# Kernel optimization log

Measured on AMD Instinct MI355X. Metric: run time of the kernel, lower is better.

The kernel has to match this reference:

```python
import jax, jax.numpy as jnp
import numpy as np

B, IN, H, OUT = 4096, 1024, 2048, 1024
EPS = 1e-5  # added to std (not variance), matching the torch module


def _ln(z, a, b):
    # torch.std default is unbiased (ddof=1); eps added to sigma
    mu = jnp.mean(z, axis=1, keepdims=True)
    sigma = jnp.std(z, axis=1, ddof=1, keepdims=True)
    return (z - mu) / (sigma + EPS) * a + b


def setup_inputs() -> dict:
    key = jax.random.key(0)
    ks = iter(jax.random.split(key, 40))
    W = lambda i, o: (jax.random.normal(next(ks), (o, i), jnp.float32) / np.sqrt(i)).astype(jnp.float32)
    bz = lambda o: jnp.zeros((o,), jnp.float32)
    d = {
        "inp": jax.random.normal(next(ks), (B, IN), jnp.float32),
        "h_0": jax.random.normal(next(ks), (B, H), jnp.float32),
        "c_0": jax.random.normal(next(ks), (B, H), jnp.float32),
        # h-side gate linears (H -> H)
        "Wfh": W(H, H), "bfh": bz(H), "Wih": W(H, H), "bih": bz(H),
        "Wch": W(H, H), "bch": bz(H), "Woh": W(H, H), "boh": bz(H),
        # x-side gate linears (IN -> H)
        "Wfx": W(IN, H), "bfx": bz(H), "Wix": W(IN, H), "bix": bz(H),
        "Wcx": W(IN, H), "bcx": bz(H), "Wox": W(IN, H), "box": bz(H),
        # decoder (H -> OUT)
        "Wdec": W(H, OUT), "bdec": bz(OUT),
        # LayerNormalization params (a2 ones, b2 zeros), shape (1, H)
        "ax": jnp.ones((1, H), jnp.float32), "bx": jnp.zeros((1, H), jnp.float32),
        "ah": jnp.ones((1, H), jnp.float32), "bh": jnp.zeros((1, H), jnp.float32),
        "ac": jnp.ones((1, H), jnp.float32), "bc": jnp.zeros((1, H), jnp.float32),
    }
    return d


def reference(inp, h_0, c_0,
              Wfh, bfh, Wih, bih, Wch, bch, Woh, boh,
              Wfx, bfx, Wix, bix, Wcx, bcx, Wox, box,
              Wdec, bdec, ax, bx, ah, bh, ac, bc):
    lin = lambda x, W, b: x @ W.T + b
    gate = lambda wx, bx_, wh, bh_: (_ln(lin(inp, wx, bx_), ax, bx)
                                     + _ln(lin(h_0, wh, bh_), ah, bh))
    f_g = jax.nn.sigmoid(gate(Wfx, bfx, Wfh, bfh))
    i_g = jax.nn.sigmoid(gate(Wix, bix, Wih, bih))
    c_tilda = jnp.tanh(gate(Wcx, bcx, Wch, bch))
    cx = f_g * c_0 + i_g * c_tilda
    o_g = jax.nn.sigmoid(gate(Wox, box, Woh, boh))
    hx = o_g * jnp.tanh(_ln(cx, ac, bc))
    out = lin(hx, Wdec, bdec)  # decoder applied to hidden state (vectorized over batch)
    return (out, hx, cx)
```

## Files before the change

kernel.cpp:

```cpp
#include <hip/hip_runtime.h>

#define NB   4096
#define NIN  1024
#define NH   2048
#define NOUT 1024
#define NH4  8192

typedef short short8 __attribute__((ext_vector_type(8)));
typedef float f32x4 __attribute__((ext_vector_type(4)));
typedef float f32x16 __attribute__((ext_vector_type(16)));
typedef unsigned short ushort8v __attribute__((ext_vector_type(8)));

__device__ __forceinline__ float bf2f(unsigned short u) {
  union { unsigned int i; float f; } c; c.i = ((unsigned int)u) << 16; return c.f;
}
__device__ __forceinline__ unsigned short f2bf(float f) {
  union { float f; unsigned int i; } c; c.f = f;
  unsigned int u = c.i;
  u += 0x7FFFu + ((u >> 16) & 1u);
  return (unsigned short)(u >> 16);
}
__device__ __forceinline__ float sigf(float x) { return 1.0f / (1.0f + __expf(-x)); }
__device__ __forceinline__ float tanh_f(float x) { return 1.0f - 2.0f / (__expf(2.0f * x) + 1.0f); }

#define CNT_INP  ((size_t)NB * NIN)
#define CNT_H0   ((size_t)NB * NH)
#define CNT_WXG  ((size_t)NH * NIN)
#define CNT_WHG  ((size_t)NH * NH)
#define CNT_WD   ((size_t)NOUT * NH)
#define OFF_XB   ((size_t)0)
#define OFF_H0B  (OFF_XB + CNT_INP)
#define OFF_HXB  (OFF_H0B + CNT_H0)
#define OFF_WX   (OFF_HXB + CNT_H0)
#define OFF_WH   (OFF_WX + 4 * CNT_WXG)
#define OFF_WD   (OFF_WH + 4 * CNT_WHG)
#define OFF_ZX   (OFF_WD + CNT_WD)
#define OFF_ZH   (OFF_ZX + (size_t)NB * NH4)
#define CVT_TOTAL (OFF_WD + CNT_WD)

struct CvtArgs { const float* src[11]; };

__global__ __launch_bounds__(256) void cvt_all(CvtArgs a, unsigned short* __restrict__ dstBase) {
  const size_t i = ((size_t)blockIdx.x * 256 + threadIdx.x) * 8;
  if (i >= CVT_TOTAL) return;
  const size_t cnt[11] = {CNT_INP, CNT_H0, CNT_WXG, CNT_WXG, CNT_WXG, CNT_WXG,
                          CNT_WHG, CNT_WHG, CNT_WHG, CNT_WHG, CNT_WD};
  const size_t dst[11] = {OFF_XB, OFF_H0B,
                          OFF_WX, OFF_WX + CNT_WXG, OFF_WX + 2 * CNT_WXG, OFF_WX + 3 * CNT_WXG,
                          OFF_WH, OFF_WH + CNT_WHG, OFF_WH + 2 * CNT_WHG, OFF_WH + 3 * CNT_WHG,
                          OFF_WD};
  size_t base = 0;
#pragma unroll
  for (int s = 0; s < 11; s++) {
    if (i < base + cnt[s]) {
      const size_t off = i - base;
      const float* sp = a.src[s] + off;
      float4 v0 = *(const float4*)(sp);
      float4 v1 = *(const float4*)(sp + 4);
      ushort8v o;
      o[0] = f2bf(v0.x); o[1] = f2bf(v0.y); o[2] = f2bf(v0.z); o[3] = f2bf(v0.w);
      o[4] = f2bf(v1.x); o[5] = f2bf(v1.y); o[6] = f2bf(v1.z); o[7] = f2bf(v1.w);
      *(ushort8v*)(dstBase + dst[s] + off) = o;
      return;
    }
    base += cnt[s];
  }
}

__device__ __forceinline__ void gload16(const void* g, void* l) {
  __builtin_amdgcn_global_load_lds((const __attribute__((address_space(1))) void*)g,
                                   (__attribute__((address_space(3))) void*)l, 16, 0, 0);
}

template<int MT, bool BOUT>
__device__ __forceinline__ void gemm_core32(const unsigned short* __restrict__ A,
                                            const unsigned short* __restrict__ Bm,
                                            const float* b0p, const float* b1p,
                                            const float* b2p, const float* b3p,
                                            float* __restrict__ Cf, unsigned short* __restrict__ Cb,
                                            int N, int K) {
  constexpr int TM = MT * 64;
  __shared__ __align__(16) unsigned short As[TM * 64];
  __shared__ __align__(16) unsigned short Bs[128 * 64];
  const int t = threadIdx.x;
  const int w = t >> 6;
  const int lane = t & 63;
  const int r31 = lane & 31;
  const int hi = lane >> 5;
  const int rloc = lane >> 3;
  const int slot = lane & 7;
  const int m0 = blockIdx.y * TM;
  const int n0 = blockIdx.x * 128;
  const int wm = (w >> 1) * (MT * 32);
  const int wn = (w & 1) * 64;

  f32x16 acc[MT][2];
#pragma unroll
  for (int i = 0; i < MT; i++)
#pragma unroll
    for (int j = 0; j < 2; j++)
#pragma unroll
      for (int r = 0; r < 16; r++) acc[i][j][r] = 0.f;

  const unsigned short* AgP[2 * MT];
  unsigned short* AsP[2 * MT];
#pragma unroll
  for (int q = 0; q < 2 * MT; q++) {
    const int iss = w + 4 * q;
    const int bblk = slot ^ rloc ^ (iss & 3);
    AgP[q] = A + (size_t)(m0 + iss * 8 + rloc) * K + bblk * 8;
    AsP[q] = As + iss * 512;
  }
  const unsigned short* BgP[4];
  unsigned short* BsP[4];
#pragma unroll
  for (int q = 0; q < 4; q++) {
    const int iss = w + 4 * q;
    const int bblk = slot ^ rloc ^ (iss & 3);
    BgP[q] = Bm + (size_t)(n0 + iss * 8 + rloc) * K + bblk * 8;
    BsP[q] = Bs + iss * 512;
  }

  const int swz = (r31 & 7) ^ ((r31 >> 3) & 3);

  for (int k0 = 0; k0 < K; k0 += 64) {
#pragma unroll
    for (int q = 0; q < 2 * MT; q++) gload16(AgP[q] + k0, AsP[q]);
#pragma unroll
    for (int q = 0; q < 4; q++) gload16(BgP[q] + k0, BsP[q]);
    __syncthreads();

#pragma unroll
    for (int ks = 0; ks < 4; ks++) {
      const int phys = ((ks * 2 + hi) ^ swz) * 8;
      short8 af[MT], bf[2];
#pragma unroll
      for (int mt = 0; mt < MT; mt++) af[mt] = *(const short8*)&As[(wm + mt * 32 + r31) * 64 + phys];
#pragma unroll
      for (int jt = 0; jt < 2; jt++) bf[jt] = *(const short8*)&Bs[(wn + jt * 32 + r31) * 64 + phys];
#pragma unroll
      for (int mt = 0; mt < MT; mt++)
#pragma unroll
        for (int jt = 0; jt < 2; jt++)
          acc[mt][jt] = __builtin_amdgcn_mfma_f32_32x32x16_bf16(af[mt], bf[jt], acc[mt][jt], 0, 0, 0);
    }
    __syncthreads();
  }

#pragma unroll
  for (int mt = 0; mt < MT; mt++) {
#pragma unroll
    for (int jt = 0; jt < 2; jt++) {
      const int col = n0 + wn + jt * 32 + r31;
      const float* bp = (col < 2048) ? b0p : ((col < 4096) ? b1p : ((col < 6144) ? b2p : b3p));
      const float bv = bp[col & 2047];
      const int rowb = m0 + wm + mt * 32 + hi * 4;
#pragma unroll
      for (int reg = 0; reg < 16; reg++) {
        const int row = rowb + (reg & 3) + 8 * (reg >> 2);
        const float v = acc[mt][jt][reg] + bv;
        const size_t idx = (size_t)row * N + col;
        if (BOUT) Cb[idx] = f2bf(v);
        else      Cf[idx] = v;
      }
    }
  }
}

__global__ __launch_bounds__(256) void gemm_dual(const unsigned short* __restrict__ Xb,
                                                 const unsigned short* __restrict__ Wx,
                                                 const unsigned short* __restrict__ H0b,
                                                 const unsigned short* __restrict__ Wh,
                                                 const float* bx0, const float* bx1,
                                                 const float* bx2, const float* bx3,
                                                 const float* bh0, const float* bh1,
                                                 const float* bh2, const float* bh3,
                                                 unsigned short* __restrict__ Zx,
                                                 unsigned short* __restrict__ Zh) {
  if (blockIdx.z == 0)
    gemm_core32<2, true>(Xb, Wx, bx0, bx1, bx2, bx3, nullptr, Zx, NH4, NIN);
  else
    gemm_core32<2, true>(H0b, Wh, bh0, bh1, bh2, bh3, nullptr, Zh, NH4, NH);
}

__global__ __launch_bounds__(256) void gemm_dec(const unsigned short* __restrict__ HXb,
                                                const unsigned short* __restrict__ Wd,
                                                const float* __restrict__ bdec,
                                                float* __restrict__ out) {
  gemm_core32<1, false>(HXb, Wd, bdec, bdec, bdec, bdec, out, nullptr, NOUT, NH);
}

__global__ __launch_bounds__(256) void ln_gates(const unsigned short* __restrict__ Zx,
                                                const unsigned short* __restrict__ Zh,
                                                const float* __restrict__ c0,
                                                const float* __restrict__ ax, const float* __restrict__ bx,
                                                const float* __restrict__ ah, const float* __restrict__ bh,
                                                const float* __restrict__ ac, const float* __restrict__ bc,
                                                float* __restrict__ out_top,
                                                unsigned short* __restrict__ hx_bf) {
  const int b = blockIdx.x;
  const int t = threadIdx.x;
  const int n = t * 8;
  const int w = t >> 6;
  const int lane = t & 63;
  const float inv_n = 1.0f / 2048.0f, inv_nm1 = 1.0f / 2047.0f;

  short8 zx[4], zh[4];
  const size_t rowoff = (size_t)b * NH4;
#pragma unroll
  for (int g = 0; g < 4; g++) {
    zx[g] = *(const short8*)(Zx + rowoff + g * NH + n);
    zh[g] = *(const short8*)(Zh + rowoff + g * NH + n);
  }

  float s[16];
#pragma unroll
  for (int g = 0; g < 4; g++) {
    float su = 0, sq = 0, su2 = 0, sq2 = 0;
#pragma unroll
    for (int j = 0; j < 8; j++) {
      float v = bf2f((unsigned short)zx[g][j]); su += v; sq += v * v;
      float u = bf2f((unsigned short)zh[g][j]); su2 += u; sq2 += u * u;
    }
    s[g * 4 + 0] = su; s[g * 4 + 1] = sq; s[g * 4 + 2] = su2; s[g * 4 + 3] = sq2;
  }
#pragma unroll
  for (int i = 0; i < 16; i++) {
    float v = s[i];
#pragma unroll
    for (int o = 32; o > 0; o >>= 1) v += __shfl_xor(v, o, 64);
    s[i] = v;
  }
  __shared__ float red[4][16];
  __shared__ float red2[4][2];
  if (lane == 0) {
#pragma unroll
    for (int i = 0; i < 16; i++) red[w][i] = s[i];
  }
  __syncthreads();
#pragma unroll
  for (int i = 0; i < 16; i++) s[i] = red[0][i] + red[1][i] + red[2][i] + red[3][i];

  float mux[4], ivx[4], muh[4], ivh[4];
#pragma unroll
  for (int g = 0; g < 4; g++) {
    mux[g] = s[g * 4 + 0] * inv_n;
    float vx = fmaxf((s[g * 4 + 1] - s[g * 4 + 0] * mux[g]) * inv_nm1, 0.0f);
    ivx[g] = 1.0f / (sqrtf(vx) + 1e-5f);
    muh[g] = s[g * 4 + 2] * inv_n;
    float vh = fmaxf((s[g * 4 + 3] - s[g * 4 + 2] * muh[g]) * inv_nm1, 0.0f);
    ivh[g] = 1.0f / (sqrtf(vh) + 1e-5f);
  }

  float axl[8], bxl[8], ahl[8], bhl[8], c0l[8];
  *(float4*)&axl[0] = *(const float4*)(ax + n); *(float4*)&axl[4] = *(const float4*)(ax + n + 4);
  *(float4*)&bxl[0] = *(const float4*)(bx + n); *(float4*)&bxl[4] = *(const float4*)(bx + n + 4);
  *(float4*)&ahl[0] = *(const float4*)(ah + n); *(float4*)&ahl[4] = *(const float4*)(ah + n + 4);
  *(float4*)&bhl[0] = *(const float4*)(bh + n); *(float4*)&bhl[4] = *(const float4*)(bh + n + 4);
  const float* c0p = c0 + (size_t)b * NH + n;
  *(float4*)&c0l[0] = *(const float4*)(c0p); *(float4*)&c0l[4] = *(const float4*)(c0p + 4);

  float cx[8], og[8];
  float cs = 0, css = 0;
#pragma unroll
  for (int j = 0; j < 8; j++) {
    float pre[4];
#pragma unroll
    for (int g = 0; g < 4; g++) {
      float vx = bf2f((unsigned short)zx[g][j]);
      float vh = bf2f((unsigned short)zh[g][j]);
      pre[g] = ((vx - mux[g]) * ivx[g]) * axl[j] + bxl[j]
             + ((vh - muh[g]) * ivh[g]) * ahl[j] + bhl[j];
    }
    float fg = sigf(pre[0]);
    float ig = sigf(pre[1]);
    float ct = tanh_f(pre[2]);
    og[j] = sigf(pre[3]);
    float c = fg * c0l[j] + ig * ct;
    cx[j] = c; cs += c; css += c * c;
  }
#pragma unroll
  for (int o = 32; o > 0; o >>= 1) { cs += __shfl_xor(cs, o, 64); css += __shfl_xor(css, o, 64); }
  if (lane == 0) { red2[w][0] = cs; red2[w][1] = css; }
  __syncthreads();
  cs = red2[0][0] + red2[1][0] + red2[2][0] + red2[3][0];
  css = red2[0][1] + red2[1][1] + red2[2][1] + red2[3][1];
  const float muc = cs * inv_n;
  const float varc = fmaxf((css - cs * muc) * inv_nm1, 0.0f);
  const float ivc = 1.0f / (sqrtf(varc) + 1e-5f);

  float acl[8], bcl[8];
  *(float4*)&acl[0] = *(const float4*)(ac + n); *(float4*)&acl[4] = *(const float4*)(ac + n + 4);
  *(float4*)&bcl[0] = *(const float4*)(bc + n); *(float4*)&bcl[4] = *(const float4*)(bc + n + 4);

  float hx[8];
#pragma unroll
  for (int j = 0; j < 8; j++)
    hx[j] = og[j] * tanh_f((cx[j] - muc) * ivc * acl[j] + bcl[j]);

  float* hx_out = out_top + (size_t)NB * NOUT + (size_t)b * NH + n;
  float* cx_out = out_top + (size_t)NB * NOUT + (size_t)NB * NH + (size_t)b * NH + n;
  float4 v;
  v.x = hx[0]; v.y = hx[1]; v.z = hx[2]; v.w = hx[3]; *(float4*)(hx_out) = v;
  v.x = hx[4]; v.y = hx[5]; v.z = hx[6]; v.w = hx[7]; *(float4*)(hx_out + 4) = v;
  v.x = cx[0]; v.y = cx[1]; v.z = cx[2]; v.w = cx[3]; *(float4*)(cx_out) = v;
  v.x = cx[4]; v.y = cx[5]; v.z = cx[6]; v.w = cx[7]; *(float4*)(cx_out + 4) = v;
  ushort8v hb;
#pragma unroll
  for (int j = 0; j < 8; j++) hb[j] = f2bf(hx[j]);
  *(ushort8v*)(hx_bf + (size_t)b * NH + n) = hb;
}

extern "C" void kernel_launch(void* const* d_in, const int* in_sizes, int n_in,
                              void* d_out, int out_size, void* d_ws, size_t ws_size,
                              hipStream_t stream) {
  const float* inp = (const float*)d_in[0];
  const float* h0  = (const float*)d_in[1];
  const float* c0  = (const float*)d_in[2];
  const float* bhg[4] = {(const float*)d_in[4], (const float*)d_in[6], (const float*)d_in[8], (const float*)d_in[10]};
  const float* bxg[4] = {(const float*)d_in[12], (const float*)d_in[14], (const float*)d_in[16], (const float*)d_in[18]};
  const float* bdec = (const float*)d_in[20];
  const float* ax = (const float*)d_in[21];
  const float* bx = (const float*)d_in[22];
  const float* ah = (const float*)d_in[23];
  const float* bh = (const float*)d_in[24];
  const float* ac = (const float*)d_in[25];
  const float* bc = (const float*)d_in[26];

  unsigned short* wsb = (unsigned short*)d_ws;
  unsigned short* Xb   = wsb + OFF_XB;
  unsigned short* H0b  = wsb + OFF_H0B;
  unsigned short* HXb  = wsb + OFF_HXB;
  unsigned short* Wx4b = wsb + OFF_WX;
  unsigned short* Wh4b = wsb + OFF_WH;
  unsigned short* Wdb  = wsb + OFF_WD;
  unsigned short* Zx   = wsb + OFF_ZX;
  unsigned short* Zh   = wsb + OFF_ZH;

  CvtArgs ca;
  ca.src[0] = inp; ca.src[1] = h0;
  ca.src[2] = (const float*)d_in[11]; ca.src[3] = (const float*)d_in[13];
  ca.src[4] = (const float*)d_in[15]; ca.src[5] = (const float*)d_in[17];
  ca.src[6] = (const float*)d_in[3];  ca.src[7] = (const float*)d_in[5];
  ca.src[8] = (const float*)d_in[7];  ca.src[9] = (const float*)d_in[9];
  ca.src[10] = (const float*)d_in[19];
  {
    const size_t nthr = CVT_TOTAL / 8;
    cvt_all<<<dim3((unsigned)((nthr + 255) / 256)), dim3(256), 0, stream>>>(ca, wsb);
  }

  gemm_dual<<<dim3(NH4 / 128, NB / 128, 2), 256, 0, stream>>>(
      Xb, Wx4b, H0b, Wh4b,
      bxg[0], bxg[1], bxg[2], bxg[3],
      bhg[0], bhg[1], bhg[2], bhg[3],
      Zx, Zh);

  ln_gates<<<dim3(NB), 256, 0, stream>>>(Zx, Zh, c0, ax, bx, ah, bh, ac, bc, (float*)d_out, HXb);

  gemm_dec<<<dim3(NOUT / 128, NB / 64), 256, 0, stream>>>(HXb, Wdb, bdec, (float*)d_out);
}
```

Before: 564.5 us.

## Split decoder GEMM along K into four partial slices plus a reduce kernel

The decoder GEMM now splits its 2048-long K dimension into four 512-wide slices launched along grid z. Each slice writes fp32 partial products into workspace memory that is no longer needed once the gate GEMM has finished. A new reduce kernel then sums the four partials and adds the decoder bias. The hx bf16 buffer moves after Zh so it does not overlap the partials. The aim is more blocks and shorter K loops per block, at the cost of writing and re-reading 64 MB of fp32 partials and one extra kernel launch.

```diff
diff --git a/kernel.cpp b/kernel.cpp
--- a/kernel.cpp
+++ b/kernel.cpp
@@ -30,12 +30,12 @@
 #define CNT_WD   ((size_t)NOUT * NH)
 #define OFF_XB   ((size_t)0)
 #define OFF_H0B  (OFF_XB + CNT_INP)
-#define OFF_HXB  (OFF_H0B + CNT_H0)
-#define OFF_WX   (OFF_HXB + CNT_H0)
+#define OFF_WX   (OFF_H0B + CNT_H0)
 #define OFF_WH   (OFF_WX + 4 * CNT_WXG)
 #define OFF_WD   (OFF_WH + 4 * CNT_WHG)
 #define OFF_ZX   (OFF_WD + CNT_WD)
 #define OFF_ZH   (OFF_ZX + (size_t)NB * NH4)
+#define OFF_HXB  (OFF_ZH + (size_t)NB * NH4)
 #define CVT_TOTAL (OFF_WD + CNT_WD)
 
 struct CvtArgs { const float* src[11]; };
@@ -72,13 +72,13 @@
                                    (__attribute__((address_space(3))) void*)l, 16, 0, 0);
 }
 
-template<int MT, bool BOUT>
+template<int MT, bool BOUT, bool BIAS>
 __device__ __forceinline__ void gemm_core32(const unsigned short* __restrict__ A,
                                             const unsigned short* __restrict__ Bm,
                                             const float* b0p, const float* b1p,
                                             const float* b2p, const float* b3p,
                                             float* __restrict__ Cf, unsigned short* __restrict__ Cb,
-                                            int N, int K) {
+                                            int N, int KL, int ld) {
   constexpr int TM = MT * 64;
   __shared__ __align__(16) unsigned short As[TM * 64];
   __shared__ __align__(16) unsigned short Bs[128 * 64];
@@ -108,7 +108,7 @@
   for (int q = 0; q < 2 * MT; q++) {
     const int iss = w + 4 * q;
     const int bblk = slot ^ rloc ^ (iss & 3);
-    AgP[q] = A + (size_t)(m0 + iss * 8 + rloc) * K + bblk * 8;
+    AgP[q] = A + (size_t)(m0 + iss * 8 + rloc) * ld + bblk * 8;
     AsP[q] = As + iss * 512;
   }
   const unsigned short* BgP[4];
@@ -117,13 +117,13 @@
   for (int q = 0; q < 4; q++) {
     const int iss = w + 4 * q;
     const int bblk = slot ^ rloc ^ (iss & 3);
-    BgP[q] = Bm + (size_t)(n0 + iss * 8 + rloc) * K + bblk * 8;
+    BgP[q] = Bm + (size_t)(n0 + iss * 8 + rloc) * ld + bblk * 8;
     BsP[q] = Bs + iss * 512;
   }
 
   const int swz = (r31 & 7) ^ ((r31 >> 3) & 3);
 
-  for (int k0 = 0; k0 < K; k0 += 64) {
+  for (int k0 = 0; k0 < KL; k0 += 64) {
 #pragma unroll
     for (int q = 0; q < 2 * MT; q++) gload16(AgP[q] + k0, AsP[q]);
 #pragma unroll
@@ -152,8 +152,11 @@
 #pragma unroll
     for (int jt = 0; jt < 2; jt++) {
       const int col = n0 + wn + jt * 32 + r31;
-      const float* bp = (col < 2048) ? b0p : ((col < 4096) ? b1p : ((col < 6144) ? b2p : b3p));
-      const float bv = bp[col & 2047];
+      float bv = 0.0f;
+      if (BIAS) {
+        const float* bp = (col < 2048) ? b0p : ((col < 4096) ? b1p : ((col < 6144) ? b2p : b3p));
+        bv = bp[col & 2047];
+      }
       const int rowb = m0 + wm + mt * 32 + hi * 4;
 #pragma unroll
       for (int reg = 0; reg < 16; reg++) {
@@ -178,16 +181,36 @@
                                                  unsigned short* __restrict__ Zx,
                                                  unsigned short* __restrict__ Zh) {
   if (blockIdx.z == 0)
-    gemm_core32<2, true>(Xb, Wx, bx0, bx1, bx2, bx3, nullptr, Zx, NH4, NIN);
+    gemm_core32<2, true, true>(Xb, Wx, bx0, bx1, bx2, bx3, nullptr, Zx, NH4, NIN, NIN);
   else
-    gemm_core32<2, true>(H0b, Wh, bh0, bh1, bh2, bh3, nullptr, Zh, NH4, NH);
+    gemm_core32<2, true, true>(H0b, Wh, bh0, bh1, bh2, bh3, nullptr, Zh, NH4, NH, NH);
 }
 
 __global__ __launch_bounds__(256) void gemm_dec(const unsigned short* __restrict__ HXb,
                                                 const unsigned short* __restrict__ Wd,
-                                                const float* __restrict__ bdec,
-                                                float* __restrict__ out) {
-  gemm_core32<1, false>(HXb, Wd, bdec, bdec, bdec, bdec, out, nullptr, NOUT, NH);
+                                                float* __restrict__ partials) {
+  const int kz = blockIdx.z;
+  gemm_core32<1, false, false>(HXb + kz * 512, Wd + kz * 512, nullptr, nullptr, nullptr, nullptr,
+                               partials + (size_t)kz * NB * NOUT, nullptr, NOUT, 512, NH);
+}
+
+__global__ __launch_bounds__(256) void dec_reduce(const float* __restrict__ partials,
+                                                  const float* __restrict__ bdec,
+                                                  float* __restrict__ out) {
+  const size_t i = ((size_t)blockIdx.x * 256 + threadIdx.x) * 4;
+  const size_t total = (size_t)NB * NOUT;
+  if (i >= total) return;
+  float4 p0 = *(const float4*)(partials + i);
+  float4 p1 = *(const float4*)(partials + total + i);
+  float4 p2 = *(const float4*)(partials + 2 * total + i);
+  float4 p3 = *(const float4*)(partials + 3 * total + i);
+  float4 bv = *(const float4*)(bdec + (i & (NOUT - 1)));
+  float4 r;
+  r.x = p0.x + p1.x + p2.x + p3.x + bv.x;
+  r.y = p0.y + p1.y + p2.y + p3.y + bv.y;
+  r.z = p0.z + p1.z + p2.z + p3.z + bv.z;
+  r.w = p0.w + p1.w + p2.w + p3.w + bv.w;
+  *(float4*)(out + i) = r;
 }
 
 __global__ __launch_bounds__(256) void ln_gates(const unsigned short* __restrict__ Zx,
@@ -330,12 +353,13 @@
   unsigned short* wsb = (unsigned short*)d_ws;
   unsigned short* Xb   = wsb + OFF_XB;
   unsigned short* H0b  = wsb + OFF_H0B;
-  unsigned short* HXb  = wsb + OFF_HXB;
   unsigned short* Wx4b = wsb + OFF_WX;
   unsigned short* Wh4b = wsb + OFF_WH;
   unsigned short* Wdb  = wsb + OFF_WD;
   unsigned short* Zx   = wsb + OFF_ZX;
   unsigned short* Zh   = wsb + OFF_ZH;
+  unsigned short* HXb  = wsb + OFF_HXB;
+  float* Pp = (float*)d_ws;
 
   CvtArgs ca;
   ca.src[0] = inp; ca.src[1] = h0;
@@ -357,5 +381,7 @@
 
   ln_gates<<<dim3(NB), 256, 0, stream>>>(Zx, Zh, c0, ax, bx, ah, bh, ac, bc, (float*)d_out, HXb);
 
-  gemm_dec<<<dim3(NOUT / 128, NB / 64), 256, 0, stream>>>(HXb, Wdb, bdec, (float*)d_out);
-}
+  gemm_dec<<<dim3(NOUT / 128, NB / 64, 4), 256, 0, stream>>>(HXb, Wdb, Pp);
+  dec_reduce<<<dim3((unsigned)(((size_t)NB * NOUT / 4 + 255) / 256)), 256, 0, stream>>>(
+      Pp, bdec, (float*)d_out);
+}
```

Measured after the change: 575.3 us. No clear change (+1.9%).
